# Performance work log

Hardware: AMD Instinct MI355X
Metric: run time of the kernel (lower is better)

Reference implementation:

```python
import jax, jax.numpy as jnp
import numpy as np

N = 131072      # nodes
E = 2097152     # edges (avg in-degree ~16)
H = 128         # hidden_dim
OUT = 128       # out_dim
G = 8192        # number of graphs in batch
A = 28          # num_atom_type
L = 4           # layers


def setup_inputs() -> dict:
    key = jax.random.key(0)
    ks = jax.random.split(key, 12)
    h = jax.random.uniform(ks[0], (N, A), dtype=jnp.float32)
    src = jax.random.randint(ks[1], (E,), 0, N, dtype=jnp.int32)
    dst = jax.random.randint(ks[2], (E,), 0, N, dtype=jnp.int32)
    graph_id = jnp.sort(jax.random.randint(ks[3], (N,), 0, G, dtype=jnp.int32))
    # snorm_n = 1/sqrt(|V_g|) per node (graph_norm)
    gcnt = jax.ops.segment_sum(jnp.ones((N,), jnp.float32), graph_id, num_segments=G)
    snorm_n = (1.0 / jnp.sqrt(jnp.maximum(gcnt, 1.0)))[graph_id][:, None]
    # parameters (Bayesian linears treated as sampled fixed weights)
    W_emb = jax.random.normal(ks[4], (A, H), jnp.float32) / np.sqrt(A)
    W_node = jax.random.normal(ks[5], (L, 2 * H, H), jnp.float32) / np.sqrt(2 * H)
    b_node = jnp.zeros((L, H), jnp.float32)
    W_ro = jax.random.normal(ks[6], (H, OUT), jnp.float32) / np.sqrt(H)
    W_pred = jax.random.normal(ks[7], (OUT, 1), jnp.float32) / np.sqrt(OUT)
    b_pred = jnp.zeros((1,), jnp.float32)
    return {"h": h, "snorm_n": snorm_n, "W_emb": W_emb, "W_node": W_node,
            "b_node": b_node, "W_ro": W_ro, "W_pred": W_pred, "b_pred": b_pred,
            "src": src, "dst": dst, "graph_id": graph_id}


def reference(h, snorm_n, W_emb, W_node, b_node, W_ro, W_pred, b_pred, src, dst, graph_id):
    # in-degree for mean aggregation (constant per graph)
    deg = jax.ops.segment_sum(jnp.ones((E,), h.dtype), dst, num_segments=N)
    inv_deg = (1.0 / jnp.maximum(deg, 1.0))[:, None]
    # per-graph node counts for mean readout
    gcnt = jax.ops.segment_sum(jnp.ones((N,), h.dtype), graph_id, num_segments=G)
    inv_gcnt = (1.0 / jnp.maximum(gcnt, 1.0))[:, None]

    h = h @ W_emb  # input embedding (dropout = identity in eval)
    for l in range(L):
        h_in = h
        # mean aggregation of in-neighbor features: c[v] = mean_{u->v} h[u]
        c = jax.ops.segment_sum(h[src], dst, num_segments=N) * inv_deg
        # NodeApply: relu(Linear([h || c]))
        h = jax.nn.relu(jnp.concatenate([h, c], axis=1) @ W_node[l] + b_node[l])
        h = h * snorm_n          # graph_norm
        h = h + h_in             # residual
    h = h @ W_ro                 # linear_ro (no bias)
    hg = jax.ops.segment_sum(h, graph_id, num_segments=G) * inv_gcnt  # mean readout
    return hg @ W_pred + b_pred  # linear_predict -> [G, 1]
```

## Files before the change

kernel.cpp:

```cpp
#include <hip/hip_runtime.h>

constexpr int NN  = 131072;
constexpr int NE  = 2097152;
constexpr int HD  = 128;
constexpr int NG  = 8192;
constexpr int NA  = 28;
constexpr int NL  = 4;

constexpr int NB   = 256;
constexpr int BSH  = 9;
constexpr int BNOD = 512;
constexpr int CAP  = 10240;

constexpr size_t SZ_FB   = (size_t)NN * HD * 2;
constexpr size_t OFF_XB   = 0;
constexpr size_t OFF_YB   = OFF_XB + SZ_FB;
constexpr size_t OFF_PB   = OFF_YB + SZ_FB;
constexpr size_t OFF_ESRC = OFF_PB + SZ_FB;
constexpr size_t OFF_DEG  = OFF_ESRC + (size_t)NE * 4;
constexpr size_t OFF_GCNT = OFF_DEG + (size_t)NN * 4;
constexpr size_t OFF_ROW  = OFF_GCNT + (size_t)NG * 4;
constexpr size_t OFF_IDEG = OFF_ROW + (size_t)NN * 4;
constexpr size_t OFF_IGC  = OFF_IDEG + (size_t)NN * 4;
constexpr size_t OFF_WC   = OFF_IGC + (size_t)NG * 4;
constexpr size_t OFF_WNT  = OFF_WC + 512;
constexpr size_t OFF_EBUF = OFF_WNT + (size_t)NL * HD * 256 * 2;
constexpr size_t OFF_GCUR = OFF_EBUF + (size_t)NB * CAP * 4;
constexpr size_t OFF_WET  = OFF_GCUR + (size_t)NB * 4;

__device__ __forceinline__ float blo(uint x) { return __uint_as_float(x << 16); }
__device__ __forceinline__ float bhi(uint x) { return __uint_as_float(x & 0xFFFF0000u); }
__device__ __forceinline__ unsigned short f2b(float f) {
  uint u = __float_as_uint(f);
  return (unsigned short)((u + 0x7FFFu + ((u >> 16) & 1u)) >> 16);
}
__device__ __forceinline__ uint pack2(float a, float b) {
  uint ua = __float_as_uint(a), ub = __float_as_uint(b);
  uint lo = (ua + 0x7FFFu + ((ua >> 16) & 1u)) >> 16;
  uint hi = (ub + 0x7FFFu + ((ub >> 16) & 1u)) & 0xFFFF0000u;
  return lo | hi;
}

typedef __attribute__((ext_vector_type(8))) short bf16x8;
typedef __attribute__((ext_vector_type(4))) float f32x4;
typedef __attribute__((ext_vector_type(2))) float f32x2;

__device__ __forceinline__ uint pk_fp8x4(float a, float b, float c, float d) {
  int p = __builtin_amdgcn_cvt_pk_fp8_f32(a, b, 0, false);
  p = __builtin_amdgcn_cvt_pk_fp8_f32(c, d, p, true);
  return (uint)p;
}

__global__ void k_ghist(const int* __restrict__ gid, int* __restrict__ gcnt) {
  int i = blockIdx.x * blockDim.x + threadIdx.x;
  if (i < NN) atomicAdd(&gcnt[gid[i]], 1);
}

__global__ void k_prep(int* __restrict__ gcur, const int* __restrict__ gcnt,
                       float* __restrict__ inv_gcnt, float* __restrict__ out,
                       const float* __restrict__ b_pred,
                       const float* __restrict__ Wn, unsigned short* __restrict__ Wnt,
                       const float* __restrict__ We, unsigned short* __restrict__ Wet,
                       const float* __restrict__ W_ro, const float* __restrict__ W_pred,
                       float* __restrict__ wcv) {
  int bi = blockIdx.x, t = threadIdx.x;
  if (bi == 0) {
    gcur[t] = t * CAP;
  } else if (bi < 1 + NG / 256) {
    int g = (bi - 1) * 256 + t;
    inv_gcnt[g] = 1.0f / fmaxf((float)gcnt[g], 1.0f);
    out[g] = b_pred[0];
  } else if (bi < 1 + NG / 256 + 512) {
    int i = (bi - 1 - NG / 256) * 256 + t;
    int l = i >> 15, k = (i >> 7) & 255, c = i & 127;
    Wnt[((size_t)l * HD + c) * 256 + k] = f2b(Wn[((size_t)l * 256 + k) * HD + c]);
  } else if (bi < 1 + NG / 256 + 512 + 16) {
    int i = (bi - 1 - NG / 256 - 512) * 256 + t;
    int col = i >> 5, k = i & 31;
    Wet[i] = (k < NA) ? f2b(We[(size_t)k * HD + col]) : (unsigned short)0;
  } else {
    if (t < 128) {
      float a = 0.f;
      for (int j = 0; j < HD; j++) a += W_ro[t * HD + j] * W_pred[j];
      wcv[t] = a;
    }
  }
}

__global__ __launch_bounds__(256) void k_bin(const int* __restrict__ src,
                                             const int* __restrict__ dst,
                                             int* __restrict__ gcur,
                                             uint* __restrict__ ebuf) {
  __shared__ int cnt[NB];
  __shared__ int gbase[NB];
  int t = threadIdx.x;
  cnt[t] = 0;
  int es[16], ed[16];
  int base = blockIdx.x * 4096 + t;
#pragma unroll
  for (int j = 0; j < 16; j++) {
    es[j] = src[base + j * 256];
    ed[j] = dst[base + j * 256];
  }
  __syncthreads();
#pragma unroll
  for (int j = 0; j < 16; j++) atomicAdd(&cnt[ed[j] >> BSH], 1);
  __syncthreads();
  int c = cnt[t];
  if (c > 0) gbase[t] = atomicAdd(&gcur[t], c);
  cnt[t] = 0;
  __syncthreads();
#pragma unroll
  for (int j = 0; j < 16; j++) {
    int b = ed[j] >> BSH;
    int r = atomicAdd(&cnt[b], 1);
    ebuf[(size_t)gbase[b] + r] = ((uint)(ed[j] & (BNOD - 1)) << 17) | (uint)es[j];
  }
}

__global__ __launch_bounds__(256) void k_csr(const int* __restrict__ gcur,
                                             const uint* __restrict__ ebuf,
                                             int* __restrict__ deg,
                                             int* __restrict__ row_start,
                                             float* __restrict__ inv_deg,
                                             int* __restrict__ esrc) {
  __shared__ int h[BNOD];
  __shared__ int ps[NB];
  __shared__ int bs[NB];
  int b = blockIdx.x, t = threadIdx.x;

  bs[t] = gcur[t] - t * CAP;
  h[t] = 0; h[t + 256] = 0;
  __syncthreads();
  for (int o = 1; o < 256; o <<= 1) {
    int v = (t >= o) ? bs[t - o] : 0;
    __syncthreads();
    bs[t] += v;
    __syncthreads();
  }
  int boff = (b == 0) ? 0 : bs[b - 1];
  int n = gcur[b] - b * CAP;

  const uint* eb = ebuf + (size_t)b * CAP;
  for (int i = t; i < n; i += 256) atomicAdd(&h[eb[i] >> 17], 1);
  __syncthreads();

  int d0 = h[2 * t], d1 = h[2 * t + 1];
  ps[t] = d0 + d1;
  __syncthreads();
  for (int o = 1; o < 256; o <<= 1) {
    int v = (t >= o) ? ps[t - o] : 0;
    __syncthreads();
    ps[t] += v;
    __syncthreads();
  }
  int excl = ps[t] - (d0 + d1);
  int r0 = boff + excl, r1 = r0 + d0;
  int v0 = b * BNOD + 2 * t;
  deg[v0] = d0;  deg[v0 + 1] = d1;
  row_start[v0] = r0;  row_start[v0 + 1] = r1;
  inv_deg[v0]     = 1.0f / fmaxf((float)d0, 1.0f);
  inv_deg[v0 + 1] = 1.0f / fmaxf((float)d1, 1.0f);
  __syncthreads();
  h[2 * t] = r0;  h[2 * t + 1] = r1;
  __syncthreads();
  for (int i = t; i < n; i += 256) {
    uint p = eb[i];
    int r = atomicAdd(&h[p >> 17], 1);
    esrc[r] = (int)(p & 0x1FFFFu);
  }
}

__global__ __launch_bounds__(256) void k_embed(const float* __restrict__ h,
                                               const unsigned short* __restrict__ Wet,
                                               unsigned short* __restrict__ Xb) {
  int t = threadIdx.x;
  int lane = t & 63, w = t >> 6;
  int wr = w >> 1, wc = w & 1;
  int row0 = blockIdx.x * 64 + wr * 32;
  int col0 = wc * 64;
  int fr = lane & 15;
  int fk = (lane >> 4) * 8;

  f32x4 acc[2][4] = {};
  bf16x8 a[2];
#pragma unroll
  for (int rt = 0; rt < 2; rt++) {
    int row = row0 + rt * 16 + fr;
    const float* hp = h + (size_t)row * NA + fk;
    float4 p = *(const float4*)hp;
    float4 q = make_float4(0.f, 0.f, 0.f, 0.f);
    if (fk < 24) q = *(const float4*)(hp + 4);
    a[rt][0] = (short)f2b(p.x); a[rt][1] = (short)f2b(p.y);
    a[rt][2] = (short)f2b(p.z); a[rt][3] = (short)f2b(p.w);
    a[rt][4] = (short)f2b(q.x); a[rt][5] = (short)f2b(q.y);
    a[rt][6] = (short)f2b(q.z); a[rt][7] = (short)f2b(q.w);
  }
#pragma unroll
  for (int ct = 0; ct < 4; ct++) {
    int col = col0 + ct * 16 + fr;
    bf16x8 b = *(const bf16x8*)(Wet + (size_t)col * 32 + fk);
#pragma unroll
    for (int rt = 0; rt < 2; rt++)
      acc[rt][ct] = __builtin_amdgcn_mfma_f32_16x16x32_bf16(a[rt], b, acc[rt][ct], 0, 0, 0);
  }
  int oc = lane & 15, orb = (lane >> 4) * 4;
#pragma unroll
  for (int rt = 0; rt < 2; rt++) {
#pragma unroll
    for (int ct = 0; ct < 4; ct++) {
      int col = col0 + ct * 16 + oc;
#pragma unroll
      for (int r = 0; r < 4; r++) {
        int row = row0 + rt * 16 + orb + r;
        Xb[(size_t)row * HD + col] = f2b(acc[rt][ct][r]);
      }
    }
  }
}

__global__ __launch_bounds__(256) void k_pq(const unsigned short* __restrict__ Hb,
                                            uint* __restrict__ Pb8,
                                            unsigned short* __restrict__ Qb,
                                            const unsigned short* __restrict__ Wt,
                                            const float* __restrict__ bias) {
  int t = threadIdx.x;
  int lane = t & 63, w = t >> 6;
  int ng = w >> 1, cg = w & 1;
  int fr = lane & 15, fkg = lane >> 4;
  int n0 = blockIdx.x * 64 + ng * 32;

  f32x4 accQ[2][4] = {}, accP[2][4] = {};
#pragma unroll
  for (int ks = 0; ks < 4; ks++) {
    bf16x8 aH[2];
#pragma unroll
    for (int nt = 0; nt < 2; nt++)
      aH[nt] = *(const bf16x8*)(Hb + (size_t)(n0 + nt * 16 + fr) * HD + ks * 32 + fkg * 8);
#pragma unroll
    for (int ct = 0; ct < 4; ct++) {
      const unsigned short* wrow =
          Wt + (size_t)(cg * 64 + ct * 16 + fr) * 256 + ks * 32 + fkg * 8;
      bf16x8 b1 = *(const bf16x8*)wrow;
      bf16x8 b2 = *(const bf16x8*)(wrow + 128);
#pragma unroll
      for (int nt = 0; nt < 2; nt++) {
        accQ[nt][ct] = __builtin_amdgcn_mfma_f32_16x16x32_bf16(b1, aH[nt], accQ[nt][ct], 0, 0, 0);
        accP[nt][ct] = __builtin_amdgcn_mfma_f32_16x16x32_bf16(b2, aH[nt], accP[nt][ct], 0, 0, 0);
      }
    }
  }
#pragma unroll
  for (int nt = 0; nt < 2; nt++) {
    int node = n0 + nt * 16 + fr;
#pragma unroll
    for (int ct = 0; ct < 4; ct++) {
      int c0 = cg * 64 + ct * 16 + fkg * 4;
      float4 bv = *(const float4*)(bias + c0);
      uint2 q;
      q.x = pack2(accQ[nt][ct][0] + bv.x, accQ[nt][ct][1] + bv.y);
      q.y = pack2(accQ[nt][ct][2] + bv.z, accQ[nt][ct][3] + bv.w);
      *(uint2*)(Qb + (size_t)node * HD + c0) = q;
      Pb8[(size_t)node * 32 + (c0 >> 2)] =
          pk_fp8x4(accP[nt][ct][0], accP[nt][ct][1], accP[nt][ct][2], accP[nt][ct][3]);
    }
  }
}

__global__ __launch_bounds__(256) void k_gapply(const uint2* __restrict__ Pg,
                      const uint4* __restrict__ Qg, const uint4* __restrict__ Hres,
                      uint4* __restrict__ Og,
                      const int* __restrict__ row_start, const int* __restrict__ deg,
                      const int* __restrict__ esrc, const float* __restrict__ inv_deg,
                      const float* __restrict__ snorm,
                      const float* __restrict__ wcv, const int* __restrict__ gid,
                      const float* __restrict__ inv_gcnt, float* __restrict__ out,
                      int last) {
  int v = blockIdx.x * 4 + (threadIdx.x >> 6);
  int lane = threadIdx.x & 63;
  int eg = lane >> 4;
  int cl = lane & 15;
  int rs = __builtin_amdgcn_readfirstlane(row_start[v]);
  int d  = __builtin_amdgcn_readfirstlane(deg[v]);

  float id = inv_deg[v];
  float sn = snorm[v];
  uint4 q  = Qg[(size_t)v * 16 + cl];
  uint4 hr = Hres[(size_t)v * 16 + cl];

  int dcap = min(d, 64);
  int myidx = 0;
  if (lane < dcap) myidx = esrc[rs + lane];

  float a0 = 0.f, a1 = 0.f, a2 = 0.f, a3 = 0.f;
  float a4 = 0.f, a5 = 0.f, a6 = 0.f, a7 = 0.f;

#define ACCX(X)                                                             \
  { f32x2 p0 = __builtin_amdgcn_cvt_pk_f32_fp8((int)(X).x, false);          \
    f32x2 p1 = __builtin_amdgcn_cvt_pk_f32_fp8((int)(X).x, true);           \
    f32x2 p2 = __builtin_amdgcn_cvt_pk_f32_fp8((int)(X).y, false);          \
    f32x2 p3 = __builtin_amdgcn_cvt_pk_f32_fp8((int)(X).y, true);           \
    a0 += p0[0]; a1 += p0[1]; a2 += p1[0]; a3 += p1[1];                     \
    a4 += p2[0]; a5 += p2[1]; a6 += p3[0]; a7 += p3[1]; }

  int e = 0;
  for (; e + 16 <= dcap; e += 16) {
    int i0 = __shfl(myidx, e + eg, 64);
    int i1 = __shfl(myidx, e + 4 + eg, 64);
    int i2 = __shfl(myidx, e + 8 + eg, 64);
    int i3 = __shfl(myidx, e + 12 + eg, 64);
    uint2 x0 = Pg[(size_t)i0 * 16 + cl];
    uint2 x1 = Pg[(size_t)i1 * 16 + cl];
    uint2 x2 = Pg[(size_t)i2 * 16 + cl];
    uint2 x3 = Pg[(size_t)i3 * 16 + cl];
    ACCX(x0)
    ACCX(x1)
    ACCX(x2)
    ACCX(x3)
  }
  if (e + 8 <= dcap) {
    int i0 = __shfl(myidx, e + eg, 64);
    int i1 = __shfl(myidx, e + 4 + eg, 64);
    uint2 x0 = Pg[(size_t)i0 * 16 + cl];
    uint2 x1 = Pg[(size_t)i1 * 16 + cl];
    ACCX(x0)
    ACCX(x1)
    e += 8;
  }
  if (e + 4 <= dcap) {
    int i0 = __shfl(myidx, e + eg, 64);
    uint2 x = Pg[(size_t)i0 * 16 + cl];
    ACCX(x)
    e += 4;
  }
  if (e < dcap) {
    uint2 x = make_uint2(0u, 0u);
    if (e + eg < dcap) {
      int i0 = __shfl(myidx, e + eg, 64);
      x = Pg[(size_t)i0 * 16 + cl];
    }
    ACCX(x)
  }
  for (int ee = 64; ee < d; ee += 4) {
    uint2 x = make_uint2(0u, 0u);
    if (ee + eg < d) x = Pg[(size_t)esrc[rs + ee + eg] * 16 + cl];
    ACCX(x)
  }
#undef ACCX

  a0 += __shfl_xor(a0, 16, 64);  a0 += __shfl_xor(a0, 32, 64);
  a1 += __shfl_xor(a1, 16, 64);  a1 += __shfl_xor(a1, 32, 64);
  a2 += __shfl_xor(a2, 16, 64);  a2 += __shfl_xor(a2, 32, 64);
  a3 += __shfl_xor(a3, 16, 64);  a3 += __shfl_xor(a3, 32, 64);
  a4 += __shfl_xor(a4, 16, 64);  a4 += __shfl_xor(a4, 32, 64);
  a5 += __shfl_xor(a5, 16, 64);  a5 += __shfl_xor(a5, 32, 64);
  a6 += __shfl_xor(a6, 16, 64);  a6 += __shfl_xor(a6, 32, 64);
  a7 += __shfl_xor(a7, 16, 64);  a7 += __shfl_xor(a7, 32, 64);

  if (eg == 0) {
    float o0 = fmaxf(blo(q.x) + a0 * id, 0.f) * sn + blo(hr.x);
    float o1 = fmaxf(bhi(q.x) + a1 * id, 0.f) * sn + bhi(hr.x);
    float o2 = fmaxf(blo(q.y) + a2 * id, 0.f) * sn + blo(hr.y);
    float o3 = fmaxf(bhi(q.y) + a3 * id, 0.f) * sn + bhi(hr.y);
    float o4 = fmaxf(blo(q.z) + a4 * id, 0.f) * sn + blo(hr.z);
    float o5 = fmaxf(bhi(q.z) + a5 * id, 0.f) * sn + bhi(hr.z);
    float o6 = fmaxf(blo(q.w) + a6 * id, 0.f) * sn + blo(hr.w);
    float o7 = fmaxf(bhi(q.w) + a7 * id, 0.f) * sn + bhi(hr.w);
    if (!last) {
      uint4 o;
      o.x = pack2(o0, o1);
      o.y = pack2(o2, o3);
      o.z = pack2(o4, o5);
      o.w = pack2(o6, o7);
      Og[(size_t)v * 16 + cl] = o;
    } else {
      float4 w0 = *(const float4*)(wcv + 8 * cl);
      float4 w1 = *(const float4*)(wcv + 8 * cl + 4);
      float p = o0 * w0.x + o1 * w0.y + o2 * w0.z + o3 * w0.w
              + o4 * w1.x + o5 * w1.y + o6 * w1.z + o7 * w1.w;
      p += __shfl_xor(p, 8, 64);
      p += __shfl_xor(p, 4, 64);
      p += __shfl_xor(p, 2, 64);
      p += __shfl_xor(p, 1, 64);
      if (cl == 0) {
        int g = gid[v];
        atomicAdd(&out[g], p * inv_gcnt[g]);
      }
    }
  }
}

extern "C" void kernel_launch(void* const* d_in, const int* in_sizes, int n_in,
                              void* d_out, int out_size, void* d_ws, size_t ws_size,
                              hipStream_t stream) {
  const float* h      = (const float*)d_in[0];
  const float* snorm  = (const float*)d_in[1];
  const float* W_emb  = (const float*)d_in[2];
  const float* W_node = (const float*)d_in[3];
  const float* b_node = (const float*)d_in[4];
  const float* W_ro   = (const float*)d_in[5];
  const float* W_pred = (const float*)d_in[6];
  const float* b_pred = (const float*)d_in[7];
  const int*   src    = (const int*)d_in[8];
  const int*   dst    = (const int*)d_in[9];
  const int*   gid    = (const int*)d_in[10];
  float* out = (float*)d_out;

  char* ws = (char*)d_ws;
  unsigned short* Xb   = (unsigned short*)(ws + OFF_XB);
  unsigned short* Yb   = (unsigned short*)(ws + OFF_YB);
  uint*  Pb8      = (uint*)(ws + OFF_PB);
  int*   esrc     = (int*)(ws + OFF_ESRC);
  int*   deg      = (int*)(ws + OFF_DEG);
  int*   gcnt     = (int*)(ws + OFF_GCNT);
  int*   row_s    = (int*)(ws + OFF_ROW);
  float* inv_deg  = (float*)(ws + OFF_IDEG);
  float* inv_gcnt = (float*)(ws + OFF_IGC);
  float* wcv      = (float*)(ws + OFF_WC);
  unsigned short* Wnt = (unsigned short*)(ws + OFF_WNT);
  uint*  ebuf     = (uint*)(ws + OFF_EBUF);
  int*   gcur     = (int*)(ws + OFF_GCUR);
  unsigned short* Wet = (unsigned short*)(ws + OFF_WET);

  hipMemsetAsync(ws + OFF_GCNT, 0, (size_t)NG * 4, stream);

  k_ghist<<<NN / 256, 256, 0, stream>>>(gid, gcnt);
  k_prep<<<1 + NG / 256 + 512 + 16 + 1, 256, 0, stream>>>(
      gcur, gcnt, inv_gcnt, out, b_pred, W_node, Wnt, W_emb, Wet, W_ro, W_pred, wcv);
  k_bin<<<NE / 4096, 256, 0, stream>>>(src, dst, gcur, ebuf);
  k_csr<<<NB, 256, 0, stream>>>(gcur, ebuf, deg, row_s, inv_deg, esrc);

  k_embed<<<NN / 64, 256, 0, stream>>>(h, Wet, Xb);

  for (int l = 0; l < NL; l++) {
    unsigned short* hb = (l & 1) ? Yb : Xb;
    unsigned short* qo = (l & 1) ? Xb : Yb;
    k_pq<<<NN / 64, 256, 0, stream>>>(hb, Pb8, qo, Wnt + (size_t)l * HD * 256,
                                      b_node + (size_t)l * HD);
    k_gapply<<<NN / 4, 256, 0, stream>>>((const uint2*)Pb8, (const uint4*)qo,
                                         (const uint4*)hb, (uint4*)qo,
                                         row_s, deg, esrc, inv_deg, snorm,
                                         wcv, gid, inv_gcnt, out, (l == NL - 1) ? 1 : 0);
  }
}
```

Measured before the change: 539.4 us.

## Process two destination nodes per wavefront in gather-apply kernel

Each wavefront in the aggregation kernel now handles two destination nodes, with each half of the wave loading the edge indices for one node. The loop issues eight independent fp8 row gathers per iteration, raising memory-level parallelism, and halves the grid. With an average in-degree near 16, the old one-node-per-wave scheme left most of the 64-lane index load idle. The trade-offs are more registers (launch bounds now request 4 waves) and divergence when the two nodes have unequal degrees.

```diff
diff --git a/kernel.cpp b/kernel.cpp
--- a/kernel.cpp
+++ b/kernel.cpp
@@ -267,7 +267,7 @@
   }
 }
 
-__global__ __launch_bounds__(256) void k_gapply(const uint2* __restrict__ Pg,
+__global__ __launch_bounds__(256, 4) void k_gapply(const uint2* __restrict__ Pg,
                       const uint4* __restrict__ Qg, const uint4* __restrict__ Hres,
                       uint4* __restrict__ Og,
                       const int* __restrict__ row_start, const int* __restrict__ deg,
@@ -276,96 +276,105 @@
                       const float* __restrict__ wcv, const int* __restrict__ gid,
                       const float* __restrict__ inv_gcnt, float* __restrict__ out,
                       int last) {
-  int v = blockIdx.x * 4 + (threadIdx.x >> 6);
+  int w = threadIdx.x >> 6;
   int lane = threadIdx.x & 63;
+  int va = blockIdx.x * 8 + w * 2;
+  int vb = va + 1;
   int eg = lane >> 4;
   int cl = lane & 15;
-  int rs = __builtin_amdgcn_readfirstlane(row_start[v]);
-  int d  = __builtin_amdgcn_readfirstlane(deg[v]);
-
-  float id = inv_deg[v];
-  float sn = snorm[v];
-  uint4 q  = Qg[(size_t)v * 16 + cl];
-  uint4 hr = Hres[(size_t)v * 16 + cl];
-
-  int dcap = min(d, 64);
+
+  int rsa = __builtin_amdgcn_readfirstlane(row_start[va]);
+  int da  = __builtin_amdgcn_readfirstlane(deg[va]);
+  int rsb = __builtin_amdgcn_readfirstlane(row_start[vb]);
+  int db  = __builtin_amdgcn_readfirstlane(deg[vb]);
+
+  float ida = inv_deg[va], idb = inv_deg[vb];
+  float sna = snorm[va],  snb = snorm[vb];
+  uint4 qa  = Qg[(size_t)va * 16 + cl];
+  uint4 qb  = Qg[(size_t)vb * 16 + cl];
+  uint4 hra = Hres[(size_t)va * 16 + cl];
+  uint4 hrb = Hres[(size_t)vb * 16 + cl];
+
+  int half = lane >> 5, l32 = lane & 31;
+  int dxa = min(da, 32), dxb = min(db, 32);
+  int rsx = half ? rsb : rsa;
+  int dxx = half ? dxb : dxa;
   int myidx = 0;
-  if (lane < dcap) myidx = esrc[rs + lane];
-
-  float a0 = 0.f, a1 = 0.f, a2 = 0.f, a3 = 0.f;
-  float a4 = 0.f, a5 = 0.f, a6 = 0.f, a7 = 0.f;
-
-#define ACCX(X)                                                             \
+  if (l32 < dxx) myidx = esrc[rsx + l32];
+
+  float Aa[8] = {}, Ab[8] = {};
+
+#define ACC8(ACC, X)                                                        \
   { f32x2 p0 = __builtin_amdgcn_cvt_pk_f32_fp8((int)(X).x, false);          \
     f32x2 p1 = __builtin_amdgcn_cvt_pk_f32_fp8((int)(X).x, true);           \
     f32x2 p2 = __builtin_amdgcn_cvt_pk_f32_fp8((int)(X).y, false);          \
     f32x2 p3 = __builtin_amdgcn_cvt_pk_f32_fp8((int)(X).y, true);           \
-    a0 += p0[0]; a1 += p0[1]; a2 += p1[0]; a3 += p1[1];                     \
-    a4 += p2[0]; a5 += p2[1]; a6 += p3[0]; a7 += p3[1]; }
-
-  int e = 0;
-  for (; e + 16 <= dcap; e += 16) {
-    int i0 = __shfl(myidx, e + eg, 64);
-    int i1 = __shfl(myidx, e + 4 + eg, 64);
-    int i2 = __shfl(myidx, e + 8 + eg, 64);
-    int i3 = __shfl(myidx, e + 12 + eg, 64);
-    uint2 x0 = Pg[(size_t)i0 * 16 + cl];
-    uint2 x1 = Pg[(size_t)i1 * 16 + cl];
-    uint2 x2 = Pg[(size_t)i2 * 16 + cl];
-    uint2 x3 = Pg[(size_t)i3 * 16 + cl];
-    ACCX(x0)
-    ACCX(x1)
-    ACCX(x2)
-    ACCX(x3)
-  }
-  if (e + 8 <= dcap) {
-    int i0 = __shfl(myidx, e + eg, 64);
-    int i1 = __shfl(myidx, e + 4 + eg, 64);
-    uint2 x0 = Pg[(size_t)i0 * 16 + cl];
-    uint2 x1 = Pg[(size_t)i1 * 16 + cl];
-    ACCX(x0)
-    ACCX(x1)
-    e += 8;
-  }
-  if (e + 4 <= dcap) {
-    int i0 = __shfl(myidx, e + eg, 64);
-    uint2 x = Pg[(size_t)i0 * 16 + cl];
-    ACCX(x)
-    e += 4;
-  }
-  if (e < dcap) {
+    ACC[0] += p0[0]; ACC[1] += p0[1]; ACC[2] += p1[0]; ACC[3] += p1[1];     \
+    ACC[4] += p2[0]; ACC[5] += p2[1]; ACC[6] += p3[0]; ACC[7] += p3[1]; }
+
+  int dmax = max(dxa, dxb);
+  for (int e = 0; e < dmax; e += 16) {
+    uint2 xa[4], xb[4];
+#pragma unroll
+    for (int j = 0; j < 4; j++) {
+      xa[j] = make_uint2(0u, 0u);
+      int ia = __shfl(myidx, e + 4 * j + eg, 64);
+      if (e + 4 * j + eg < dxa) xa[j] = Pg[(size_t)ia * 16 + cl];
+    }
+#pragma unroll
+    for (int j = 0; j < 4; j++) {
+      xb[j] = make_uint2(0u, 0u);
+      int ib = __shfl(myidx, 32 + e + 4 * j + eg, 64);
+      if (e + 4 * j + eg < dxb) xb[j] = Pg[(size_t)ib * 16 + cl];
+    }
+#pragma unroll
+    for (int j = 0; j < 4; j++) ACC8(Aa, xa[j])
+#pragma unroll
+    for (int j = 0; j < 4; j++) ACC8(Ab, xb[j])
+  }
+  for (int ee = 32; ee < da; ee += 4) {
     uint2 x = make_uint2(0u, 0u);
-    if (e + eg < dcap) {
-      int i0 = __shfl(myidx, e + eg, 64);
-      x = Pg[(size_t)i0 * 16 + cl];
-    }
-    ACCX(x)
-  }
-  for (int ee = 64; ee < d; ee += 4) {
+    if (ee + eg < da) x = Pg[(size_t)esrc[rsa + ee + eg] * 16 + cl];
+    ACC8(Aa, x)
+  }
+  for (int ee = 32; ee < db; ee += 4) {
     uint2 x = make_uint2(0u, 0u);
-    if (ee + eg < d) x = Pg[(size_t)esrc[rs + ee + eg] * 16 + cl];
-    ACCX(x)
-  }
-#undef ACCX
-
-  a0 += __shfl_xor(a0, 16, 64);  a0 += __shfl_xor(a0, 32, 64);
-  a1 += __shfl_xor(a1, 16, 64);  a1 += __shfl_xor(a1, 32, 64);
-  a2 += __shfl_xor(a2, 16, 64);  a2 += __shfl_xor(a2, 32, 64);
-  a3 += __shfl_xor(a3, 16, 64);  a3 += __shfl_xor(a3, 32, 64);
-  a4 += __shfl_xor(a4, 16, 64);  a4 += __shfl_xor(a4, 32, 64);
-  a5 += __shfl_xor(a5, 16, 64);  a5 += __shfl_xor(a5, 32, 64);
-  a6 += __shfl_xor(a6, 16, 64);  a6 += __shfl_xor(a6, 32, 64);
-  a7 += __shfl_xor(a7, 16, 64);  a7 += __shfl_xor(a7, 32, 64);
-
-  if (eg == 0) {
-    float o0 = fmaxf(blo(q.x) + a0 * id, 0.f) * sn + blo(hr.x);
-    float o1 = fmaxf(bhi(q.x) + a1 * id, 0.f) * sn + bhi(hr.x);
-    float o2 = fmaxf(blo(q.y) + a2 * id, 0.f) * sn + blo(hr.y);
-    float o3 = fmaxf(bhi(q.y) + a3 * id, 0.f) * sn + bhi(hr.y);
-    float o4 = fmaxf(blo(q.z) + a4 * id, 0.f) * sn + blo(hr.z);
-    float o5 = fmaxf(bhi(q.z) + a5 * id, 0.f) * sn + bhi(hr.z);
-    float o6 = fmaxf(blo(q.w) + a6 * id, 0.f) * sn + blo(hr.w);
-    float o7 = fmaxf(bhi(q.w) + a7 * id, 0.f) * sn + bhi(hr.w);
+    if (ee + eg < db) x = Pg[(size_t)esrc[rsb + ee + eg] * 16 + cl];
+    ACC8(Ab, x)
+  }
+#undef ACC8
+
+#pragma unroll
+  for (int i = 0; i < 8; i++) {
+    Aa[i] += __shfl_xor(Aa[i], 16, 64);
+    Aa[i] += __shfl_xor(Aa[i], 32, 64);
+    Ab[i] += __shfl_xor(Ab[i], 16, 64);
+    Ab[i] += __shfl_xor(Ab[i], 32, 64);
+  }
+
+  if (eg < 2) {
+    bool isA = (eg == 0);
+    int v    = isA ? va : vb;
+    float id = isA ? ida : idb;
+    float sn = isA ? sna : snb;
+    uint4 q  = isA ? qa : qb;
+    uint4 hr = isA ? hra : hrb;
+    float s0 = isA ? Aa[0] : Ab[0];
+    float s1 = isA ? Aa[1] : Ab[1];
+    float s2 = isA ? Aa[2] : Ab[2];
+    float s3 = isA ? Aa[3] : Ab[3];
+    float s4 = isA ? Aa[4] : Ab[4];
+    float s5 = isA ? Aa[5] : Ab[5];
+    float s6 = isA ? Aa[6] : Ab[6];
+    float s7 = isA ? Aa[7] : Ab[7];
+    float o0 = fmaxf(blo(q.x) + s0 * id, 0.f) * sn + blo(hr.x);
+    float o1 = fmaxf(bhi(q.x) + s1 * id, 0.f) * sn + bhi(hr.x);
+    float o2 = fmaxf(blo(q.y) + s2 * id, 0.f) * sn + blo(hr.y);
+    float o3 = fmaxf(bhi(q.y) + s3 * id, 0.f) * sn + bhi(hr.y);
+    float o4 = fmaxf(blo(q.z) + s4 * id, 0.f) * sn + blo(hr.z);
+    float o5 = fmaxf(bhi(q.z) + s5 * id, 0.f) * sn + bhi(hr.z);
+    float o6 = fmaxf(blo(q.w) + s6 * id, 0.f) * sn + blo(hr.w);
+    float o7 = fmaxf(bhi(q.w) + s7 * id, 0.f) * sn + bhi(hr.w);
     if (!last) {
       uint4 o;
       o.x = pack2(o0, o1);
@@ -437,7 +446,7 @@
     unsigned short* qo = (l & 1) ? Xb : Yb;
     k_pq<<<NN / 64, 256, 0, stream>>>(hb, Pb8, qo, Wnt + (size_t)l * HD * 256,
                                       b_node + (size_t)l * HD);
-    k_gapply<<<NN / 4, 256, 0, stream>>>((const uint2*)Pb8, (const uint4*)qo,
+    k_gapply<<<NN / 8, 256, 0, stream>>>((const uint2*)Pb8, (const uint4*)qo,
                                          (const uint4*)hb, (uint4*)qo,
                                          row_s, deg, esrc, inv_deg, snorm,
                                          wcv, gid, inv_gcnt, out, (l == NL - 1) ? 1 : 0);
```

Measured after the change: 569.6 us. 1.06x slower.
